# Optimization experiments

Measured on AMD Instinct MI355X. Metric: run time of the kernel, lower is better.

The kernel has to match this reference:

```python
import jax, jax.numpy as jnp
import numpy as np

D_MODEL = 1024
H = 16
D_K = D_MODEL // H
B, S = 2, 2048


def setup_inputs() -> dict:
    key = jax.random.key(0)
    ks = jax.random.split(key, 13)
    sc = 1.0 / np.sqrt(D_MODEL)
    inp = {
        "x": jax.random.normal(ks[0], (B, S, D_MODEL), jnp.float32),
        "q": jax.random.normal(ks[1], (B, S, D_MODEL), jnp.float32),
        "k": jax.random.normal(ks[2], (B, S, D_MODEL), jnp.float32),
        "v": jax.random.normal(ks[3], (B, S, D_MODEL), jnp.float32),
        "mask": jnp.ones((1, 1, S, S), jnp.int32),
        "w_q": jax.random.normal(ks[4], (D_MODEL, D_MODEL), jnp.float32) * sc,
        "b_q": jax.random.normal(ks[5], (D_MODEL,), jnp.float32) * sc,
        "w_k": jax.random.normal(ks[6], (D_MODEL, D_MODEL), jnp.float32) * sc,
        "b_k": jax.random.normal(ks[7], (D_MODEL,), jnp.float32) * sc,
        "w_v": jax.random.normal(ks[8], (D_MODEL, D_MODEL), jnp.float32) * sc,
        "b_v": jax.random.normal(ks[9], (D_MODEL,), jnp.float32) * sc,
        "w_o": jax.random.normal(ks[10], (D_MODEL, D_MODEL), jnp.float32) * sc,
        "b_o": jax.random.normal(ks[11], (D_MODEL,), jnp.float32) * sc,
    }
    return inp


def reference(x, q, k, v, mask, w_q, b_q, w_k, b_k, w_v, b_v, w_o, b_o):
    # Faithful to source bugs: value projected with w_k (not w_v);
    # mask and dropout have no effect (non-in-place / broken calls); x unused.
    query = q @ w_q.T + b_q                     # [B,S,D]
    key_p = k @ w_k.T + b_k                     # [B,S,D]
    value = v @ w_k.T + b_k                     # BUG in source: uses w_k
    # split heads -> [B,H,S,d_k]
    qh = query.reshape(B, S, H, D_K).transpose(0, 2, 1, 3)
    kh = key_p.reshape(B, S, H, D_K).transpose(0, 2, 1, 3)
    vh = value.reshape(B, S, H, D_K).transpose(0, 2, 1, 3)
    scores = jnp.einsum("bhqd,bhkd->bhqk", qh, kh) / jnp.sqrt(jnp.float32(D_K))
    attn = jax.nn.softmax(scores, axis=-1)      # [B,H,S,S]
    out = jnp.einsum("bhqk,bhkd->bhqd", attn, vh)
    out = out.transpose(0, 2, 1, 3).reshape(B, S, D_MODEL)
    return out @ w_o.T + b_o
```

## Files before the change

### kernel.cpp

```cpp
#include <hip/hip_runtime.h>

typedef unsigned short u16;
typedef __attribute__((ext_vector_type(8))) __bf16 bf16x8;
typedef __attribute__((ext_vector_type(4))) float f32x4;
typedef __attribute__((ext_vector_type(16))) float f32x16;
typedef __attribute__((ext_vector_type(8))) u16 u16x8;
typedef __attribute__((ext_vector_type(4))) u16 u16x4;
typedef __attribute__((ext_vector_type(4))) unsigned u32x4;

#define AS1 __attribute__((address_space(1)))
#define AS3 __attribute__((address_space(3)))

#if __has_builtin(__builtin_amdgcn_exp2f)
#define EXP2(x) __builtin_amdgcn_exp2f(x)
#else
#define EXP2(x) exp2f(x)
#endif

__device__ __forceinline__ u16 f2bf(float f) {
  union { float f; unsigned u; } cv; cv.f = f;
  return (u16)((cv.u + 0x7FFFu + ((cv.u >> 16) & 1u)) >> 16);
}

__device__ __forceinline__ void gload16(const void* g, void* l) {
  __builtin_amdgcn_global_load_lds((AS1 const void*)g, (AS3 void*)l, 16, 0, 0);
}

__device__ __forceinline__ unsigned cvtpk(float lo, float hi_) {
  unsigned d;
  asm("v_cvt_pk_bf16_f32 %0, %1, %2" : "=v"(d) : "v"(lo), "v"(hi_));
  return d;
}

__device__ __forceinline__ int lds_off(int row, int chunk) {
  return row * 64 + ((chunk ^ (row & 7)) << 3);
}

__global__ void cvt_kernel(const float* __restrict__ s0, u16* __restrict__ d0, int n0,
                           const float* __restrict__ s1, u16* __restrict__ d1, int n1,
                           const float* __restrict__ s2, u16* __restrict__ d2, int n2,
                           const float* __restrict__ s3, u16* __restrict__ d3, int n3,
                           const float* __restrict__ s4, u16* __restrict__ d4, int n4,
                           const float* __restrict__ s5, u16* __restrict__ d5, int n5) {
  const float* s; u16* d; int n;
  switch (blockIdx.y) {
    case 0: s = s0; d = d0; n = n0; break;
    case 1: s = s1; d = d1; n = n1; break;
    case 2: s = s2; d = d2; n = n2; break;
    case 3: s = s3; d = d3; n = n3; break;
    case 4: s = s4; d = d4; n = n4; break;
    default: s = s5; d = d5; n = n5; break;
  }
  const int stride = gridDim.x * blockDim.x;
  for (int i = blockIdx.x * blockDim.x + threadIdx.x; i < n; i += stride) {
    const float4* p = (const float4*)(s + (size_t)i * 8);
    float4 a = p[0], b = p[1];
    u16x8 r;
    r[0] = f2bf(a.x); r[1] = f2bf(a.y); r[2] = f2bf(a.z); r[3] = f2bf(a.w);
    r[4] = f2bf(b.x); r[5] = f2bf(b.y); r[6] = f2bf(b.z); r[7] = f2bf(b.w);
    *(u16x8*)(d + (size_t)i * 8) = r;
  }
}

__device__ __forceinline__ void gemm_core(const u16* __restrict__ A,
                                          const u16* __restrict__ Bm,
                                          u16* As, u16* Bs,
                                          int rowBase, int colBase,
                                          f32x4 acc[4][4]) {
  const int tid = threadIdx.x;
  const int lane = tid & 63, w = tid >> 6;
  const int wr = w >> 1, wc = w & 1;
  const int l15 = lane & 15, g = lane >> 4;

  for (int kt = 0; kt < 1024; kt += 32) {
    __syncthreads();
#pragma unroll
    for (int it = 0; it < 2; ++it) {
      int e = it * 256 + tid;
      int r = e >> 2, kc = (e & 3) << 3;
      gload16(A + (((size_t)(rowBase + r)) << 10) + kt + kc, As + e * 8);
      gload16(Bm + (((size_t)(colBase + r)) << 10) + kt + kc, Bs + e * 8);
    }
    __syncthreads();
    bf16x8 a[4], b[4];
#pragma unroll
    for (int mt = 0; mt < 4; ++mt)
      a[mt] = *(const bf16x8*)(As + (wr * 64 + mt * 16 + l15) * 32 + g * 8);
#pragma unroll
    for (int nt = 0; nt < 4; ++nt)
      b[nt] = *(const bf16x8*)(Bs + (wc * 64 + nt * 16 + l15) * 32 + g * 8);
#pragma unroll
    for (int mt = 0; mt < 4; ++mt)
#pragma unroll
      for (int nt = 0; nt < 4; ++nt)
        acc[mt][nt] = __builtin_amdgcn_mfma_f32_16x16x32_bf16(a[mt], b[nt], acc[mt][nt], 0, 0, 0);
  }
}

__global__ __launch_bounds__(256)
void proj_gemm(const u16* __restrict__ qb, const u16* __restrict__ kb, const u16* __restrict__ vb,
               const u16* __restrict__ wqb, const u16* __restrict__ wkb,
               const float* __restrict__ b_q, const float* __restrict__ b_k,
               u16* __restrict__ Qp, u16* __restrict__ Kp, u16* __restrict__ VTp) {
  __shared__ __align__(16) u16 As[128 * 32];
  __shared__ __align__(16) u16 Bs[128 * 32];

  const u16* A; const u16* Bm; const float* bias; u16* C; int mode;
  float scale = 1.0f;
  if (blockIdx.z == 0)      { A = qb; Bm = wqb; bias = b_q; C = Qp;  mode = 0; scale = 0.18033688011112042f; }
  else if (blockIdx.z == 1) { A = kb; Bm = wkb; bias = b_k; C = Kp;  mode = 0; }
  else                      { A = vb; Bm = wkb; bias = b_k; C = VTp; mode = 1; }

  const int rowBase = blockIdx.x * 128;
  const int colBase = blockIdx.y * 128;
  f32x4 acc[4][4];
  const f32x4 z4 = {0.f, 0.f, 0.f, 0.f};
#pragma unroll
  for (int i = 0; i < 4; ++i)
#pragma unroll
    for (int j = 0; j < 4; ++j) acc[i][j] = z4;

  gemm_core(A, Bm, As, Bs, rowBase, colBase, acc);

  const int tid = threadIdx.x;
  const int lane = tid & 63, w = tid >> 6;
  const int wr = w >> 1, wc = w & 1;
  const int l15 = lane & 15, g = lane >> 4;
#pragma unroll
  for (int mt = 0; mt < 4; ++mt)
#pragma unroll
    for (int nt = 0; nt < 4; ++nt) {
      int col = colBase + wc * 64 + nt * 16 + l15;
      float bia = bias[col];
#pragma unroll
      for (int r = 0; r < 4; ++r) {
        int row = rowBase + wr * 64 + mt * 16 + g * 4 + r;
        float val = (acc[mt][nt][r] + bia) * scale;
        if (mode == 0) {
          C[(((size_t)row) << 10) + col] = f2bf(val);
        } else {
          int bb = row >> 11, s = row & 2047;
          int s2 = s ^ ((((s >> 2) ^ (s >> 3)) & 1) * 12);
          int hh = col >> 6, d = col & 63;
          C[((((size_t)(bb * 16 + hh)) << 6) + d) * 2048 + s2] = f2bf(val);
        }
      }
    }
}

__global__ __launch_bounds__(256)
void out_gemm(const u16* __restrict__ AO, const u16* __restrict__ wob,
              const float* __restrict__ b_o, float* __restrict__ C) {
  __shared__ __align__(16) u16 As[64 * 32];
  __shared__ __align__(16) u16 Bs[128 * 32];
  const int rowBase = blockIdx.x * 64;
  const int colBase = blockIdx.y * 128;

  const int tid = threadIdx.x;
  const int lane = tid & 63, w = tid >> 6;
  const int wr = w >> 1, wc = w & 1;
  const int l15 = lane & 15, g = lane >> 4;

  f32x4 acc[2][4];
  const f32x4 z4 = {0.f, 0.f, 0.f, 0.f};
#pragma unroll
  for (int i = 0; i < 2; ++i)
#pragma unroll
    for (int j = 0; j < 4; ++j) acc[i][j] = z4;

  for (int kt = 0; kt < 1024; kt += 32) {
    __syncthreads();
    {
      int r = tid >> 2, kc = (tid & 3) << 3;
      gload16(AO + (((size_t)(rowBase + r)) << 10) + kt + kc, As + tid * 8);
    }
#pragma unroll
    for (int it = 0; it < 2; ++it) {
      int e = it * 256 + tid;
      int r = e >> 2, kc = (e & 3) << 3;
      gload16(wob + (((size_t)(colBase + r)) << 10) + kt + kc, Bs + e * 8);
    }
    __syncthreads();
    bf16x8 a[2], b[4];
#pragma unroll
    for (int mt = 0; mt < 2; ++mt)
      a[mt] = *(const bf16x8*)(As + (wr * 32 + mt * 16 + l15) * 32 + g * 8);
#pragma unroll
    for (int nt = 0; nt < 4; ++nt)
      b[nt] = *(const bf16x8*)(Bs + (wc * 64 + nt * 16 + l15) * 32 + g * 8);
#pragma unroll
    for (int mt = 0; mt < 2; ++mt)
#pragma unroll
      for (int nt = 0; nt < 4; ++nt)
        acc[mt][nt] = __builtin_amdgcn_mfma_f32_16x16x32_bf16(a[mt], b[nt], acc[mt][nt], 0, 0, 0);
  }

#pragma unroll
  for (int mt = 0; mt < 2; ++mt)
#pragma unroll
    for (int nt = 0; nt < 4; ++nt) {
      int col = colBase + wc * 64 + nt * 16 + l15;
      float bia = b_o[col];
#pragma unroll
      for (int r = 0; r < 4; ++r) {
        int row = rowBase + wr * 32 + mt * 16 + g * 4 + r;
        C[(((size_t)row) << 10) + col] = acc[mt][nt][r] + bia;
      }
    }
}

template <int KS4>
__device__ __forceinline__ void pv_step(const f32x16& sv, int hi, const u16* Vt, int l31,
                                        f32x16& o0, f32x16& o1) {
  constexpr int B = (KS4 & 1) * 8;
  u32x4 pd;
  pd[0] = cvtpk(sv[B + 0], sv[B + 1]);
  pd[1] = cvtpk(sv[B + 2], sv[B + 3]);
  pd[2] = cvtpk(sv[B + 4], sv[B + 5]);
  pd[3] = cvtpk(sv[B + 6], sv[B + 7]);
  bf16x8 pfrag = __builtin_bit_cast(bf16x8, pd);
  bf16x8 av0 = *(const bf16x8*)(Vt + lds_off(l31, 2 * KS4 + hi));
  bf16x8 av1 = *(const bf16x8*)(Vt + lds_off(32 + l31, 2 * KS4 + hi));
  o0 = __builtin_amdgcn_mfma_f32_32x32x16_bf16(av0, pfrag, o0, 0, 0, 0);
  o1 = __builtin_amdgcn_mfma_f32_32x32x16_bf16(av1, pfrag, o1, 0, 0, 0);
}

__global__ __launch_bounds__(256, 2)
void flash_attn(const u16* __restrict__ Qp, const u16* __restrict__ Kp,
                const u16* __restrict__ VT, u16* __restrict__ AO) {
  __shared__ __align__(16) u16 KB[2][64 * 64];
  __shared__ __align__(16) u16 VB[2][64 * 64];

  const int tid = threadIdx.x;
  const int lane = tid & 63;
  const int w = tid >> 6;
  const int l31 = lane & 31;
  const int hi = lane >> 5;

  const int flat = blockIdx.x + (blockIdx.y << 4);
  const int wgid = (flat & 7) * 64 + (flat >> 3);
  const int bh = wgid >> 4;
  const int qblk = wgid & 15;
  const int b = bh >> 4, h = bh & 15;
  const int q = qblk * 128 + w * 32 + l31;

  const size_t qrow = ((size_t)(b * 2048 + q)) << 10;
  const u16* Kbase = Kp + (((size_t)(b * 2048)) << 10) + h * 64;
  const u16* Vbase = VT + (((size_t)(bh * 64)) << 11);

  const int sr = tid >> 3;
  const int sc = (tid & 7) ^ (sr & 7);

  auto stage = [&](int tt, int buf) {
    const int kv0 = tt * 64;
    gload16(Kbase + (((size_t)(kv0 + sr)) << 10) + sc * 8, &KB[buf][tid * 8]);
    gload16(Kbase + (((size_t)(kv0 + 32 + sr)) << 10) + sc * 8, &KB[buf][2048 + tid * 8]);
    gload16(Vbase + sr * 2048 + kv0 + sc * 8, &VB[buf][tid * 8]);
    gload16(Vbase + (32 + sr) * 2048 + kv0 + sc * 8, &VB[buf][2048 + tid * 8]);
  };

  stage(0, 0);

  bf16x8 qf[4];
#pragma unroll
  for (int ks = 0; ks < 4; ++ks)
    qf[ks] = *(const bf16x8*)(Qp + qrow + h * 64 + ks * 16 + hi * 8);

  float m = -1e30f, l = 0.f;
  f32x16 o0, o1;
#pragma unroll
  for (int i = 0; i < 16; ++i) { o0[i] = 0.f; o1[i] = 0.f; }

  for (int t = 0; t < 32; ++t) {
    const int cb = t & 1;
    asm volatile("s_waitcnt vmcnt(0)" ::: "memory");
    __builtin_amdgcn_sched_barrier(0);
    __builtin_amdgcn_s_barrier();
    __builtin_amdgcn_sched_barrier(0);
    if (t < 31) stage(t + 1, cb ^ 1);

    const u16* Kt = &KB[cb][0];
    const u16* Vt = &VB[cb][0];

    f32x16 s0, s1;
#pragma unroll
    for (int i = 0; i < 16; ++i) { s0[i] = 0.f; s1[i] = 0.f; }
#pragma unroll
    for (int ks = 0; ks < 4; ++ks) {
      bf16x8 ak0 = *(const bf16x8*)(Kt + lds_off(l31, 2 * ks + hi));
      bf16x8 ak1 = *(const bf16x8*)(Kt + lds_off(32 + l31, 2 * ks + hi));
      s0 = __builtin_amdgcn_mfma_f32_32x32x16_bf16(ak0, qf[ks], s0, 0, 0, 0);
      s1 = __builtin_amdgcn_mfma_f32_32x32x16_bf16(ak1, qf[ks], s1, 0, 0, 0);
    }

    f32x16 mm;
#pragma unroll
    for (int i = 0; i < 16; ++i) mm[i] = fmaxf(s0[i], s1[i]);
#pragma unroll
    for (int i = 0; i < 8; ++i) mm[i] = fmaxf(mm[i], mm[i + 8]);
#pragma unroll
    for (int i = 0; i < 4; ++i) mm[i] = fmaxf(mm[i], mm[i + 4]);
    float pm = fmaxf(fmaxf(mm[0], mm[1]), fmaxf(mm[2], mm[3]));
    pm = fmaxf(pm, __shfl_xor(pm, 32));

    if (!__all(pm - m <= 11.0f)) {
      float mn = fmaxf(m, pm);
      float fr = EXP2(m - mn);
      m = mn;
      l *= fr;
#pragma unroll
      for (int i = 0; i < 16; ++i) { o0[i] *= fr; o1[i] *= fr; }
    }

#pragma unroll
    for (int i = 0; i < 16; ++i) {
      s0[i] = EXP2(s0[i] - m);
      s1[i] = EXP2(s1[i] - m);
    }
#pragma unroll
    for (int i = 0; i < 16; ++i) mm[i] = s0[i] + s1[i];
#pragma unroll
    for (int i = 0; i < 8; ++i) mm[i] += mm[i + 8];
#pragma unroll
    for (int i = 0; i < 4; ++i) mm[i] += mm[i + 4];
    float ps = (mm[0] + mm[1]) + (mm[2] + mm[3]);
    ps += __shfl_xor(ps, 32);
    l += ps;

    pv_step<0>(s0, hi, Vt, l31, o0, o1);
    pv_step<1>(s0, hi, Vt, l31, o0, o1);
    pv_step<2>(s1, hi, Vt, l31, o0, o1);
    pv_step<3>(s1, hi, Vt, l31, o0, o1);
  }

  const float linv = 1.0f / l;
#pragma unroll
  for (int dt = 0; dt < 2; ++dt) {
    const f32x16& oo = dt ? o1 : o0;
#pragma unroll
    for (int g = 0; g < 4; ++g) {
      u16x4 pk;
#pragma unroll
      for (int r = 0; r < 4; ++r) pk[r] = f2bf(oo[g * 4 + r] * linv);
      const int d = dt * 32 + g * 8 + hi * 4;
      *(u16x4*)(AO + qrow + h * 64 + d) = pk;
    }
  }
}

extern "C" void kernel_launch(void* const* d_in, const int* in_sizes, int n_in,
                              void* d_out, int out_size, void* d_ws, size_t ws_size,
                              hipStream_t stream) {
  const float* q   = (const float*)d_in[1];
  const float* k   = (const float*)d_in[2];
  const float* v   = (const float*)d_in[3];
  const float* w_q = (const float*)d_in[5];
  const float* b_q = (const float*)d_in[6];
  const float* w_k = (const float*)d_in[7];
  const float* b_k = (const float*)d_in[8];
  const float* w_o = (const float*)d_in[11];
  const float* b_o = (const float*)d_in[12];
  float* out = (float*)d_out;

  u16* qb  = (u16*)d_ws;
  u16* kb  = qb  + 4194304;
  u16* vb  = kb  + 4194304;
  u16* wqb = vb  + 4194304;
  u16* wkb = wqb + 1048576;
  u16* wob = wkb + 1048576;
  u16* Qp  = wob + 1048576;
  u16* Kp  = Qp  + 4194304;
  u16* VTp = Kp  + 4194304;
  u16* AO  = qb;

  cvt_kernel<<<dim3(512, 6, 1), 256, 0, stream>>>(
      q, qb, 524288, k, kb, 524288, v, vb, 524288,
      w_q, wqb, 131072, w_k, wkb, 131072, w_o, wob, 131072);

  proj_gemm<<<dim3(32, 8, 3), 256, 0, stream>>>(qb, kb, vb, wqb, wkb, b_q, b_k, Qp, Kp, VTp);

  flash_attn<<<dim3(16, 32, 1), 256, 0, stream>>>(Qp, Kp, VTp, AO);

  out_gemm<<<dim3(64, 8, 1), 256, 0, stream>>>(AO, wob, b_o, out);
}
```

Measured before the change: 128.7 us.

## Split KV sequence across two wave groups in flash attention and merge partials

Doubles the flash attention block to 512 threads, with two groups of four waves each handling half of the KV sequence (16 tiles each) for the same 128 query rows. Partial max, sum and output accumulators from the second group go through shared memory and are merged by the first group before the normalized bf16 write. The goal is more waves per CU and shorter per-wave serial loops, which should hide latency better. The cost is double the LDS per block, an extra sync and merge step, and launch bounds of 512 threads with 4 blocks that may constrain registers.

```diff
diff --git a/kernel.cpp b/kernel.cpp
--- a/kernel.cpp
+++ b/kernel.cpp
@@ -225,62 +225,66 @@
   o1 = __builtin_amdgcn_mfma_f32_32x32x16_bf16(av1, pfrag, o1, 0, 0, 0);
 }
 
-__global__ __launch_bounds__(256, 2)
+__global__ __launch_bounds__(512, 4)
 void flash_attn(const u16* __restrict__ Qp, const u16* __restrict__ Kp,
                 const u16* __restrict__ VT, u16* __restrict__ AO) {
-  __shared__ __align__(16) u16 KB[2][64 * 64];
-  __shared__ __align__(16) u16 VB[2][64 * 64];
+  __shared__ __align__(16) u16 KB[2][2][64 * 64];
+  __shared__ __align__(16) u16 VB[2][2][64 * 64];
+  __shared__ float shML[2][256];
 
   const int tid = threadIdx.x;
   const int lane = tid & 63;
   const int w = tid >> 6;
+  const int h = w >> 2;
+  const int wq = w & 3;
   const int l31 = lane & 31;
   const int hi = lane >> 5;
+  const int tid256 = tid & 255;
 
   const int flat = blockIdx.x + (blockIdx.y << 4);
   const int wgid = (flat & 7) * 64 + (flat >> 3);
   const int bh = wgid >> 4;
   const int qblk = wgid & 15;
-  const int b = bh >> 4, h = bh & 15;
-  const int q = qblk * 128 + w * 32 + l31;
+  const int b = bh >> 4, hd = bh & 15;
+  const int q = qblk * 128 + wq * 32 + l31;
 
   const size_t qrow = ((size_t)(b * 2048 + q)) << 10;
-  const u16* Kbase = Kp + (((size_t)(b * 2048)) << 10) + h * 64;
+  const u16* Kbase = Kp + (((size_t)(b * 2048)) << 10) + hd * 64;
   const u16* Vbase = VT + (((size_t)(bh * 64)) << 11);
 
-  const int sr = tid >> 3;
-  const int sc = (tid & 7) ^ (sr & 7);
+  const int sr = tid256 >> 3;
+  const int sc = (tid256 & 7) ^ (sr & 7);
 
   auto stage = [&](int tt, int buf) {
     const int kv0 = tt * 64;
-    gload16(Kbase + (((size_t)(kv0 + sr)) << 10) + sc * 8, &KB[buf][tid * 8]);
-    gload16(Kbase + (((size_t)(kv0 + 32 + sr)) << 10) + sc * 8, &KB[buf][2048 + tid * 8]);
-    gload16(Vbase + sr * 2048 + kv0 + sc * 8, &VB[buf][tid * 8]);
-    gload16(Vbase + (32 + sr) * 2048 + kv0 + sc * 8, &VB[buf][2048 + tid * 8]);
+    gload16(Kbase + (((size_t)(kv0 + sr)) << 10) + sc * 8, &KB[h][buf][tid256 * 8]);
+    gload16(Kbase + (((size_t)(kv0 + 32 + sr)) << 10) + sc * 8, &KB[h][buf][2048 + tid256 * 8]);
+    gload16(Vbase + sr * 2048 + kv0 + sc * 8, &VB[h][buf][tid256 * 8]);
+    gload16(Vbase + (32 + sr) * 2048 + kv0 + sc * 8, &VB[h][buf][2048 + tid256 * 8]);
   };
 
-  stage(0, 0);
+  stage(h * 16, 0);
 
   bf16x8 qf[4];
 #pragma unroll
   for (int ks = 0; ks < 4; ++ks)
-    qf[ks] = *(const bf16x8*)(Qp + qrow + h * 64 + ks * 16 + hi * 8);
+    qf[ks] = *(const bf16x8*)(Qp + qrow + hd * 64 + ks * 16 + hi * 8);
 
   float m = -1e30f, l = 0.f;
   f32x16 o0, o1;
 #pragma unroll
   for (int i = 0; i < 16; ++i) { o0[i] = 0.f; o1[i] = 0.f; }
 
-  for (int t = 0; t < 32; ++t) {
-    const int cb = t & 1;
+  for (int lt = 0; lt < 16; ++lt) {
+    const int cb = lt & 1;
     asm volatile("s_waitcnt vmcnt(0)" ::: "memory");
     __builtin_amdgcn_sched_barrier(0);
     __builtin_amdgcn_s_barrier();
     __builtin_amdgcn_sched_barrier(0);
-    if (t < 31) stage(t + 1, cb ^ 1);
-
-    const u16* Kt = &KB[cb][0];
-    const u16* Vt = &VB[cb][0];
+    if (lt < 15) stage(h * 16 + lt + 1, cb ^ 1);
+
+    const u16* Kt = &KB[h][cb][0];
+    const u16* Vt = &VB[h][cb][0];
 
     f32x16 s0, s1;
 #pragma unroll
@@ -333,17 +337,40 @@
     pv_step<3>(s1, hi, Vt, l31, o0, o1);
   }
 
-  const float linv = 1.0f / l;
-#pragma unroll
-  for (int dt = 0; dt < 2; ++dt) {
-    const f32x16& oo = dt ? o1 : o0;
-#pragma unroll
-    for (int g = 0; g < 4; ++g) {
-      u16x4 pk;
-#pragma unroll
-      for (int r = 0; r < 4; ++r) pk[r] = f2bf(oo[g * 4 + r] * linv);
-      const int d = dt * 32 + g * 8 + hi * 4;
-      *(u16x4*)(AO + qrow + h * 64 + d) = pk;
+  const int wl = wq * 64 + lane;
+  float* shO0 = (float*)&KB[1][0][0];
+  float* shO1 = (float*)&VB[1][0][0];
+  if (h == 1) {
+#pragma unroll
+    for (int i = 0; i < 16; ++i) {
+      shO0[i * 256 + wl] = o0[i];
+      shO1[i * 256 + wl] = o1[i];
+    }
+    shML[0][wl] = m;
+    shML[1][wl] = l;
+  }
+  __syncthreads();
+  if (h == 0) {
+    float mb = shML[0][wl], lb = shML[1][wl];
+    float M = fmaxf(m, mb);
+    float f0 = EXP2(m - M), f1 = EXP2(mb - M);
+    float linv = 1.0f / (l * f0 + lb * f1);
+#pragma unroll
+    for (int i = 0; i < 16; ++i) {
+      o0[i] = o0[i] * f0 + shO0[i * 256 + wl] * f1;
+      o1[i] = o1[i] * f0 + shO1[i * 256 + wl] * f1;
+    }
+#pragma unroll
+    for (int dt = 0; dt < 2; ++dt) {
+      const f32x16& oo = dt ? o1 : o0;
+#pragma unroll
+      for (int g = 0; g < 4; ++g) {
+        u16x4 pk;
+#pragma unroll
+        for (int r = 0; r < 4; ++r) pk[r] = f2bf(oo[g * 4 + r] * linv);
+        const int d = dt * 32 + g * 8 + hi * 4;
+        *(u16x4*)(AO + qrow + hd * 64 + d) = pk;
+      }
     }
   }
 }
@@ -379,7 +406,7 @@
 
   proj_gemm<<<dim3(32, 8, 3), 256, 0, stream>>>(qb, kb, vb, wqb, wkb, b_q, b_k, Qp, Kp, VTp);
 
-  flash_attn<<<dim3(16, 32, 1), 256, 0, stream>>>(Qp, Kp, VTp, AO);
+  flash_attn<<<dim3(16, 32, 1), 512, 0, stream>>>(Qp, Kp, VTp, AO);
 
   out_gemm<<<dim3(64, 8, 1), 256, 0, stream>>>(AO, wob, b_o, out);
 }
```

After: 125.8 us. 2.3% less time.
